# Performance work log

Hardware: AMD Instinct MI355X
Metric: run time of the kernel (lower is better)

Reference implementation:

```python
import jax, jax.numpy as jnp
import numpy as np

# ---- static config (mirrors init_kwargs + fixed setup box dims) ----
PC_MIN = jnp.array([0.0, -40.0, -3.0])
VOXEL_SIZE = jnp.array([0.05, 0.05, 0.1])
STRIDE = 4                     # pool_cfg.STRIDE and multi_scale_3d_strides['x_conv4']
EXTEND = 2.0                   # model_cfg.ROI_EXTEND_FACTOR
GRID_ZYX = (10, 400, 352)      # sparse spatial shape after stride-4 downsample [z,y,x]
# grid_size = round(extended_dims / voxel_size / STRIDE) for fixed dims [6.4,3.2,1.6]
GX, GY, GZ = 64, 32, 4
G = GX * GY * GZ
N_VOX, C = 200_000, 128
M = 64
KX, KY, KZ = 7, 7, 3


def setup_inputs() -> dict:
    key = jax.random.key(0)
    k1, k2, k3, k4, k5, k6, k7, k8, k9 = jax.random.split(key, 9)
    ctr = jnp.stack([
        jax.random.uniform(k1, (M,), minval=10.0, maxval=60.0),
        jax.random.uniform(k2, (M,), minval=-25.0, maxval=25.0),
        jax.random.uniform(k3, (M,), minval=-1.5, maxval=0.5)], axis=-1)
    dims = jnp.tile(jnp.array([[6.4, 3.2, 1.6]], jnp.float32), (M, 1))  # fixed -> static grid
    yaw = jax.random.uniform(k4, (M, 1), minval=-np.pi, maxval=np.pi)
    rois = jnp.concatenate([ctr, dims, yaw], axis=-1).astype(jnp.float32)
    proto_box = jnp.array([0.0, 0.0, 0.0, 6.4, 3.2, 1.6, 0.3], jnp.float32)
    voxel_feats = jax.random.normal(k5, (N_VOX, C), jnp.float32)
    feat_proto = jax.random.normal(k6, (1, KX, KY, KZ, C), jnp.float32) * 0.1
    zc = jax.random.randint(k7, (N_VOX,), 0, GRID_ZYX[0])
    yc = jax.random.randint(k8, (N_VOX,), 0, GRID_ZYX[1])
    xc = jax.random.randint(k9, (N_VOX,), 0, GRID_ZYX[2])
    voxel_coords = jnp.stack([jnp.zeros_like(zc), zc, yc, xc], -1).astype(jnp.int32)
    return dict(rois=rois, proto_box=proto_box, voxel_feats=voxel_feats,
                feat_proto=feat_proto, voxel_coords=voxel_coords)


def _dense_grid_points(box):
    # get_dense_grid_points: row-major (x,y,z) index order, matches torch nonzero()
    idx = jnp.stack(jnp.meshgrid(jnp.arange(GX), jnp.arange(GY), jnp.arange(GZ),
                                 indexing='ij'), -1).reshape(-1, 3).astype(jnp.float32)
    gs = jnp.array([GX, GY, GZ], jnp.float32)
    return (idx + 0.5) / gs * box[3:6] - box[3:6] / 2.0  # (G,3)


def _rotate_z(pts, ang):
    # common_utils.rotate_points_along_z: pts @ [[c,s,0],[-s,c,0],[0,0,1]]
    c, s = jnp.cos(ang), jnp.sin(ang)
    R = jnp.stack([jnp.stack([c, s, 0.0 * c]),
                   jnp.stack([-s, c, 0.0 * c]),
                   jnp.stack([0.0 * c, 0.0 * c, 1.0 + 0.0 * c])])
    return pts @ R


def reference(rois, proto_box, voxel_feats, feat_proto, voxel_coords):
    # generate_voxel2pinds: dense [Z,Y,X] grid of voxel row indices, -1 = empty
    v2p = -jnp.ones(GRID_ZYX, jnp.int32)
    v2p = v2p.at[voxel_coords[:, 1], voxel_coords[:, 2], voxel_coords[:, 3]].set(
        jnp.arange(N_VOX, dtype=jnp.int32))

    def per_roi(box):
        box = box.at[3:5].multiply(EXTEND)                 # xy_dim_extend
        local = _dense_grid_points(box)                    # (G,3)
        xyz = _rotate_z(local, box[6]) + box[:3]           # global roi grid points
        coords = jnp.floor((xyz - PC_MIN) / VOXEL_SIZE)    # '//' floor-div semantics
        coords = jnp.floor(coords / STRIDE).astype(jnp.int32)
        xc, yc, zc = coords[:, 0], coords[:, 1], coords[:, 2]
        inb = ((zc >= 0) & (zc < GRID_ZYX[0]) & (yc >= 0) & (yc < GRID_ZYX[1]) &
               (xc >= 0) & (xc < GRID_ZYX[2]))
        pidx = v2p[jnp.clip(zc, 0, GRID_ZYX[0] - 1),
                   jnp.clip(yc, 0, GRID_ZYX[1] - 1),
                   jnp.clip(xc, 0, GRID_ZYX[2] - 1)]
        valid = inb & (pidx >= 0)
        feat = jnp.where(valid[:, None], voxel_feats[jnp.clip(pidx, 0)], 0.0)  # (G,C)
        return feat, xyz

    feats, grid_xyz = jax.vmap(per_roi)(rois)              # (M,G,C), (M,G,3)
    vol = feats.reshape(M, GX, GY, GZ, C).transpose(0, 4, 1, 2, 3)   # NCDHW
    kern = feat_proto.transpose(0, 4, 1, 2, 3)                        # (1,C,KX,KY,KZ)
    pads = [(KX // 2,) * 2, (KY // 2,) * 2, (KZ // 2,) * 2]           # ceil((k-1)/2)
    mm = jax.lax.conv_general_dilated(vol, kern, (1, 1, 1), pads,
                                      dimension_numbers=('NCDHW', 'OIDHW', 'NCDHW'))
    # fresh BatchNorm3d(1) applied per-ROI (batch 1 each call): per-sample norm
    mu = jnp.mean(mm, axis=(1, 2, 3, 4), keepdims=True)
    var = jnp.var(mm, axis=(1, 2, 3, 4), keepdims=True)
    mm = (mm - mu) / jnp.sqrt(var + 1e-5)
    idx = jnp.minimum(jnp.argmax(mm.reshape(M, -1), axis=1), G - 1)
    sel = jnp.take_along_axis(grid_xyz, idx[:, None, None], axis=1)[:, 0, :]  # (M,3)
    rois_new = jnp.tile(proto_box[None], (M, 1))
    rois_new = rois_new.at[:, :3].set(sel)
    return rois_new
```

## Files before the change

kernel.cpp:

```cpp
#include <hip/hip_runtime.h>
#include <stdint.h>

#define GRID_Z 10
#define GRID_Y 400
#define GRID_X 352
#define NGRID (GRID_Z * GRID_Y * GRID_X)
#define NVOX 200000
#define CCH 128
#define MROI 64
#define GXD 64
#define GYD 32
#define GZD 4
#define GCELLS 8192
#define NTAPS 147
#define TROWS 32
#define NSLC 12
#define PITCH 136
#define NTT 10
#define BFRAGN (NTT * 4 * 64)

typedef short bf16x8 __attribute__((ext_vector_type(8)));
typedef float f32x4 __attribute__((ext_vector_type(4)));

__device__ __forceinline__ unsigned f2bf(float x) {
    unsigned u = __float_as_uint(x);
    return (u + 0x7FFFu + ((u >> 16) & 1u)) >> 16;
}
__device__ __forceinline__ float bf2f(unsigned h) {
    return __uint_as_float(h << 16);
}

__device__ __forceinline__ void cell_xyz(const float* __restrict__ roi, int g,
                                         float& X, float& Y, float& Z) {
#pragma clang fp contract(off)
    int iz = g & 3;
    int iy = (g >> 2) & 31;
    int ix = g >> 7;
    float bx = roi[3] * 2.0f;
    float by = roi[4] * 2.0f;
    float bz = roi[5];
    float lx = (ix + 0.5f) / 64.0f * bx - bx / 2.0f;
    float ly = (iy + 0.5f) / 32.0f * by - by / 2.0f;
    float lz = (iz + 0.5f) / 4.0f  * bz - bz / 2.0f;
    float c = cosf(roi[6]);
    float s = sinf(roi[6]);
    X = lx * c + ly * (-s) + roi[0];
    Y = lx * s + ly * c    + roi[1];
    Z = lz + roi[2];
}

__device__ __forceinline__ int cell_to_pidx(const float* __restrict__ roi, int g,
                                            const int* __restrict__ v2p) {
#pragma clang fp contract(off)
    float X, Y, Z;
    cell_xyz(roi, g, X, Y, Z);
    float fx = floorf((X - 0.0f)     / 0.05f);
    float fy = floorf((Y - (-40.0f)) / 0.05f);
    float fz = floorf((Z - (-3.0f))  / 0.1f);
    int cx = (int)floorf(fx / 4.0f);
    int cy = (int)floorf(fy / 4.0f);
    int cz = (int)floorf(fz / 4.0f);
    int p = -1;
    if (cz >= 0 && cz < GRID_Z && cy >= 0 && cy < GRID_Y && cx >= 0 && cx < GRID_X)
        p = v2p[(cz * GRID_Y + cy) * GRID_X + cx];
    return p;
}

__global__ void k_prep(const float* __restrict__ fproto,
                       uint4* __restrict__ bH, uint4* __restrict__ bL) {
    int tT   = blockIdx.x;
    int ks   = threadIdx.x >> 6;
    int lane = threadIdx.x & 63;
    int tap  = tT * 16 + (lane & 15);
    int k0   = ks * 32 + (lane >> 4) * 8;
    unsigned hi[8], lo[8];
    #pragma unroll
    for (int j = 0; j < 8; ++j) {
        float x = (tap < NTAPS) ? fproto[tap * CCH + k0 + j] : 0.0f;
        unsigned h = f2bf(x);
        float r = x - bf2f(h);
        hi[j] = h;
        lo[j] = f2bf(r);
    }
    uint4 uh, ul;
    uh.x = hi[0] | (hi[1] << 16); uh.y = hi[2] | (hi[3] << 16);
    uh.z = hi[4] | (hi[5] << 16); uh.w = hi[6] | (hi[7] << 16);
    ul.x = lo[0] | (lo[1] << 16); ul.y = lo[2] | (lo[3] << 16);
    ul.z = lo[4] | (lo[5] << 16); ul.w = lo[6] | (lo[7] << 16);
    int idx = (tT * 4 + ks) * 64 + lane;
    bH[idx] = uh;
    bL[idx] = ul;
}

__global__ void k_scatter(const int* __restrict__ vcoords, int* __restrict__ v2p,
                          int* __restrict__ cnt) {
    int i = blockIdx.x * 256 + threadIdx.x;
    if (blockIdx.x == 0 && threadIdx.x < MROI) cnt[threadIdx.x] = 0;
    if (i >= NVOX) return;
    int z = vcoords[i * 4 + 1];
    int y = vcoords[i * 4 + 2];
    int x = vcoords[i * 4 + 3];
    atomicMax(&v2p[(z * GRID_Y + y) * GRID_X + x], i);
}

__global__ void k_build(const float* __restrict__ rois, const int* __restrict__ v2p,
                        unsigned* __restrict__ list, int* __restrict__ cnt) {
    int g = blockIdx.x * 256 + threadIdx.x;
    int m = blockIdx.y;
    int lane = threadIdx.x & 63;
    int p = cell_to_pidx(rois + m * 7, g, v2p);
    bool v = p >= 0;
    unsigned long long bal = __ballot(v);
    int nset = __popcll(bal);
    int base = 0;
    if (lane == 0 && nset) base = atomicAdd(&cnt[m], nset);
    base = __shfl(base, 0, 64);
    if (v) {
        int pos = __popcll(bal & ((1ull << lane) - 1ull));
        list[m * GCELLS + base + pos] = ((unsigned)p << 13) | (unsigned)g;
    }
}

__global__ __launch_bounds__(256) void k_dots(
        const float* __restrict__ vfeat, const uint4* __restrict__ bH,
        const uint4* __restrict__ bL, const unsigned* __restrict__ list,
        const int* __restrict__ cnt, float* __restrict__ partial) {
    __shared__ float sscore[GCELLS];
    __shared__ __align__(16) unsigned short sAh[TROWS * PITCH];
    __shared__ __align__(16) unsigned short sAl[TROWS * PITCH];
    __shared__ unsigned sg[TROWS];

    const int m    = blockIdx.y;
    const int tid  = threadIdx.x;
    const int w    = tid >> 6;
    const int lane = tid & 63;
    const int rt   = w >> 1;
    const int th   = w & 1;
    const int col  = lane & 15;
    const int kg   = lane >> 4;
    const int n    = cnt[m];
    const unsigned* lst = list + m * GCELLS;

    int tkx[5], tky[5], tkz[5], tok[5];
    #pragma unroll
    for (int tt = 0; tt < 5; ++tt) {
        int t = th * 80 + tt * 16 + col;
        tok[tt] = t < NTAPS;
        int tc = tok[tt] ? t : 0;
        int kx  = tc / 21;
        int rem = tc - kx * 21;
        tkx[tt] = kx; tky[tt] = rem / 3; tkz[tt] = rem - tky[tt] * 3;
    }
    {
        float4* s4 = (float4*)sscore;
        #pragma unroll
        for (int i = 0; i < GCELLS / 4 / 256; ++i)
            s4[tid + 256 * i] = make_float4(0.f, 0.f, 0.f, 0.f);
    }
    for (int vt0 = blockIdx.x * TROWS; vt0 < n; vt0 += TROWS * NSLC) {
        __syncthreads();
        {
            int r = tid >> 3, q = tid & 7, v = vt0 + r;
            unsigned e = 0xFFFFFFFFu;
            if (v < n) e = lst[v];
            if (q == 0) sg[r] = e;
            if (e != 0xFFFFFFFFu) {
                int p = (int)(e >> 13);
                const float4* src = (const float4*)(vfeat + (size_t)p * CCH) + q * 4;
                unsigned hb[16], lb[16];
                #pragma unroll
                for (int j = 0; j < 4; ++j) {
                    float4 s = src[j];
                    float xs[4] = {s.x, s.y, s.z, s.w};
                    #pragma unroll
                    for (int c = 0; c < 4; ++c) {
                        unsigned h = f2bf(xs[c]);
                        hb[j * 4 + c] = h;
                        lb[j * 4 + c] = f2bf(xs[c] - bf2f(h));
                    }
                }
                uint4 h0, h1, l0, l1;
                h0.x = hb[0]  | (hb[1]  << 16); h0.y = hb[2]  | (hb[3]  << 16);
                h0.z = hb[4]  | (hb[5]  << 16); h0.w = hb[6]  | (hb[7]  << 16);
                h1.x = hb[8]  | (hb[9]  << 16); h1.y = hb[10] | (hb[11] << 16);
                h1.z = hb[12] | (hb[13] << 16); h1.w = hb[14] | (hb[15] << 16);
                l0.x = lb[0]  | (lb[1]  << 16); l0.y = lb[2]  | (lb[3]  << 16);
                l0.z = lb[4]  | (lb[5]  << 16); l0.w = lb[6]  | (lb[7]  << 16);
                l1.x = lb[8]  | (lb[9]  << 16); l1.y = lb[10] | (lb[11] << 16);
                l1.z = lb[12] | (lb[13] << 16); l1.w = lb[14] | (lb[15] << 16);
                uint4* dh = (uint4*)((char*)sAh + r * (PITCH * 2) + q * 32);
                uint4* dl = (uint4*)((char*)sAl + r * (PITCH * 2) + q * 32);
                dh[0] = h0; dh[1] = h1;
                dl[0] = l0; dl[1] = l1;
            }
        }
        __syncthreads();
        bf16x8 ah[4], al[4];
        const char* abh = (const char*)sAh + (rt * 16 + col) * (PITCH * 2);
        const char* abl = (const char*)sAl + (rt * 16 + col) * (PITCH * 2);
        #pragma unroll
        for (int ks = 0; ks < 4; ++ks) {
            ah[ks] = *(const bf16x8*)(abh + ks * 64 + kg * 16);
            al[ks] = *(const bf16x8*)(abl + ks * 64 + kg * 16);
        }
        f32x4 acc[5];
        #pragma unroll
        for (int tt = 0; tt < 5; ++tt) acc[tt] = (f32x4){0.f, 0.f, 0.f, 0.f};
        #pragma unroll
        for (int tt = 0; tt < 5; ++tt) {
            const int bi = ((th * 5 + tt) * 4) * 64 + lane;
            #pragma unroll
            for (int ks = 0; ks < 4; ++ks) {
                uint4 uh = bH[bi + ks * 64];
                uint4 ul = bL[bi + ks * 64];
                bf16x8 bh = *(bf16x8*)&uh;
                bf16x8 bl = *(bf16x8*)&ul;
                acc[tt] = __builtin_amdgcn_mfma_f32_16x16x32_bf16(ah[ks], bh, acc[tt], 0, 0, 0);
                acc[tt] = __builtin_amdgcn_mfma_f32_16x16x32_bf16(ah[ks], bl, acc[tt], 0, 0, 0);
                acc[tt] = __builtin_amdgcn_mfma_f32_16x16x32_bf16(al[ks], bh, acc[tt], 0, 0, 0);
            }
        }
        #pragma unroll
        for (int tt = 0; tt < 5; ++tt) {
            if (!tok[tt]) continue;
            #pragma unroll
            for (int rg = 0; rg < 4; ++rg) {
                unsigned e = sg[rt * 16 + kg * 4 + rg];
                if (e == 0xFFFFFFFFu) continue;
                int g  = (int)(e & 8191u);
                int cx = (g >> 7)        - (tkx[tt] - 3);
                int cy = ((g >> 2) & 31) - (tky[tt] - 3);
                int cz = (g & 3)         - (tkz[tt] - 1);
                if ((unsigned)cx < (unsigned)GXD && (unsigned)cy < (unsigned)GYD &&
                    (unsigned)cz < (unsigned)GZD)
                    atomicAdd(&sscore[(cx << 7) | (cy << 2) | cz], acc[tt][rg]);
            }
        }
    }
    __syncthreads();
    {
        float* dst = partial + ((size_t)m * NSLC + blockIdx.x) * GCELLS;
        const float4* s4 = (const float4*)sscore;
        float4* d4 = (float4*)dst;
        #pragma unroll
        for (int i = 0; i < GCELLS / 4 / 256; ++i)
            d4[tid + 256 * i] = s4[tid + 256 * i];
    }
}

__global__ __launch_bounds__(1024) void k_argfin(
        const float* __restrict__ partial, const float* __restrict__ rois,
        const float* __restrict__ pbox, float* __restrict__ out) {
    __shared__ unsigned long long red[1024];
    int m = blockIdx.x;
    int tid = threadIdx.x;
    const float* base = partial + (size_t)m * NSLC * GCELLS;
    unsigned long long bk = 0ull;
    #pragma unroll
    for (int i = 0; i < GCELLS / 1024; ++i) {
        int g = tid + 1024 * i;
        float v = 0.0f;
        #pragma unroll
        for (int s = 0; s < NSLC; ++s) v += base[s * GCELLS + g];
        unsigned ub  = __float_as_uint(v);
        unsigned key = (ub & 0x80000000u) ? ~ub : (ub | 0x80000000u);
        unsigned long long pk =
            ((unsigned long long)key << 32) | (unsigned)(GCELLS - 1 - g);
        bk = bk > pk ? bk : pk;
    }
    red[tid] = bk;
    __syncthreads();
    for (int s = 512; s > 0; s >>= 1) {
        if (tid < s) {
            unsigned long long o = red[tid + s];
            if (o > red[tid]) red[tid] = o;
        }
        __syncthreads();
    }
    if (tid == 0) {
        int g = (GCELLS - 1) - (int)(unsigned)(red[0] & 0xFFFFFFFFu);
        float X, Y, Z;
        cell_xyz(rois + m * 7, g, X, Y, Z);
        out[m * 7 + 0] = X;
        out[m * 7 + 1] = Y;
        out[m * 7 + 2] = Z;
        out[m * 7 + 3] = pbox[3];
        out[m * 7 + 4] = pbox[4];
        out[m * 7 + 5] = pbox[5];
        out[m * 7 + 6] = pbox[6];
    }
}

extern "C" void kernel_launch(void* const* d_in, const int* in_sizes, int n_in,
                              void* d_out, int out_size, void* d_ws, size_t ws_size,
                              hipStream_t stream) {
    const float* rois    = (const float*)d_in[0];
    const float* pbox    = (const float*)d_in[1];
    const float* vfeat   = (const float*)d_in[2];
    const float* fproto  = (const float*)d_in[3];
    const int*   vcoords = (const int*)d_in[4];
    float* out = (float*)d_out;

    int*      v2p     = (int*)d_ws;
    unsigned* list    = (unsigned*)(v2p + NGRID);
    float*    partial = (float*)(list + (size_t)MROI * GCELLS);
    uint4*    bH      = (uint4*)(partial + (size_t)NSLC * MROI * GCELLS);
    uint4*    bL      = bH + BFRAGN;
    int*      cnt     = (int*)(bL + BFRAGN);

    hipMemsetAsync(v2p, 0xFF, (size_t)NGRID * 4, stream);
    k_prep   <<<NTT, 256, 0, stream>>>(fproto, bH, bL);
    k_scatter<<<(NVOX + 255) / 256, 256, 0, stream>>>(vcoords, v2p, cnt);
    k_build  <<<dim3(GCELLS / 256, MROI), 256, 0, stream>>>(rois, v2p, list, cnt);
    k_dots   <<<dim3(NSLC, MROI), 256, 0, stream>>>(vfeat, bH, bL, list, cnt, partial);
    k_argfin <<<MROI, 1024, 0, stream>>>(partial, rois, pbox, out);
}
```

Before: 281.7 us.

## Fuse memset into prep kernel, hoist trig in build, split argmax across blocks

Replaces the hipMemsetAsync of the voxel-to-point map with int4 stores inside an enlarged prep kernel. That kernel also precomputes per-ROI cos/sin and resets the counters. The build kernel now has each thread handle one (x,y) column and loop over the 4 z cells, so the rotation math runs once per column. The final argmax is split across 16 blocks per ROI that merge through a global atomicMax, and the last block to finish, detected with a done counter, writes all outputs. The aim is to cut launch and serial overhead and to raise parallelism in the tail kernel, at the cost of grid-wide atomics and a last-block handoff.

```diff
diff --git a/kernel.cpp b/kernel.cpp
--- a/kernel.cpp
+++ b/kernel.cpp
@@ -18,6 +18,8 @@
 #define PITCH 136
 #define NTT 10
 #define BFRAGN (NTT * 4 * 64)
+#define VCLR ((NGRID / 4 + 255) / 256)
+#define ABLK 16
 
 typedef short bf16x8 __attribute__((ext_vector_type(8)));
 typedef float f32x4 __attribute__((ext_vector_type(4)));
@@ -49,53 +51,55 @@
     Z = lz + roi[2];
 }
 
-__device__ __forceinline__ int cell_to_pidx(const float* __restrict__ roi, int g,
-                                            const int* __restrict__ v2p) {
+__global__ void k_prep(const float* __restrict__ fproto, const float* __restrict__ rois,
+                       uint4* __restrict__ bH, uint4* __restrict__ bL,
+                       float2* __restrict__ rtrig, unsigned long long* __restrict__ best,
+                       int* __restrict__ cnt, unsigned* __restrict__ done,
+                       int* __restrict__ v2p) {
+    if (blockIdx.x < NTT) {
+        int tT   = blockIdx.x;
+        int ks   = threadIdx.x >> 6;
+        int lane = threadIdx.x & 63;
+        int tap  = tT * 16 + (lane & 15);
+        int k0   = ks * 32 + (lane >> 4) * 8;
+        unsigned hi[8], lo[8];
+        #pragma unroll
+        for (int j = 0; j < 8; ++j) {
+            float x = (tap < NTAPS) ? fproto[tap * CCH + k0 + j] : 0.0f;
+            unsigned h = f2bf(x);
+            float r = x - bf2f(h);
+            hi[j] = h;
+            lo[j] = f2bf(r);
+        }
+        uint4 uh, ul;
+        uh.x = hi[0] | (hi[1] << 16); uh.y = hi[2] | (hi[3] << 16);
+        uh.z = hi[4] | (hi[5] << 16); uh.w = hi[6] | (hi[7] << 16);
+        ul.x = lo[0] | (lo[1] << 16); ul.y = lo[2] | (lo[3] << 16);
+        ul.z = lo[4] | (lo[5] << 16); ul.w = lo[6] | (lo[7] << 16);
+        int idx = (tT * 4 + ks) * 64 + lane;
+        bH[idx] = uh;
+        bL[idx] = ul;
+    } else if (blockIdx.x == NTT) {
 #pragma clang fp contract(off)
-    float X, Y, Z;
-    cell_xyz(roi, g, X, Y, Z);
-    float fx = floorf((X - 0.0f)     / 0.05f);
-    float fy = floorf((Y - (-40.0f)) / 0.05f);
-    float fz = floorf((Z - (-3.0f))  / 0.1f);
-    int cx = (int)floorf(fx / 4.0f);
-    int cy = (int)floorf(fy / 4.0f);
-    int cz = (int)floorf(fz / 4.0f);
-    int p = -1;
-    if (cz >= 0 && cz < GRID_Z && cy >= 0 && cy < GRID_Y && cx >= 0 && cx < GRID_X)
-        p = v2p[(cz * GRID_Y + cy) * GRID_X + cx];
-    return p;
-}
-
-__global__ void k_prep(const float* __restrict__ fproto,
-                       uint4* __restrict__ bH, uint4* __restrict__ bL) {
-    int tT   = blockIdx.x;
-    int ks   = threadIdx.x >> 6;
-    int lane = threadIdx.x & 63;
-    int tap  = tT * 16 + (lane & 15);
-    int k0   = ks * 32 + (lane >> 4) * 8;
-    unsigned hi[8], lo[8];
-    #pragma unroll
-    for (int j = 0; j < 8; ++j) {
-        float x = (tap < NTAPS) ? fproto[tap * CCH + k0 + j] : 0.0f;
-        unsigned h = f2bf(x);
-        float r = x - bf2f(h);
-        hi[j] = h;
-        lo[j] = f2bf(r);
-    }
-    uint4 uh, ul;
-    uh.x = hi[0] | (hi[1] << 16); uh.y = hi[2] | (hi[3] << 16);
-    uh.z = hi[4] | (hi[5] << 16); uh.w = hi[6] | (hi[7] << 16);
-    ul.x = lo[0] | (lo[1] << 16); ul.y = lo[2] | (lo[3] << 16);
-    ul.z = lo[4] | (lo[5] << 16); ul.w = lo[6] | (lo[7] << 16);
-    int idx = (tT * 4 + ks) * 64 + lane;
-    bH[idx] = uh;
-    bL[idx] = ul;
-}
-
-__global__ void k_scatter(const int* __restrict__ vcoords, int* __restrict__ v2p,
-                          int* __restrict__ cnt) {
+        int t = threadIdx.x;
+        if (t < MROI) {
+            float yaw = rois[t * 7 + 6];
+            rtrig[t] = make_float2(cosf(yaw), sinf(yaw));
+            cnt[t] = 0;
+            best[t] = 0ull;
+        }
+        if (t == 0) *done = 0u;
+    } else {
+        int i = (blockIdx.x - NTT - 1) * 256 + threadIdx.x;
+        if (i < NGRID / 4) {
+            int4* p = (int4*)v2p;
+            p[i] = make_int4(-1, -1, -1, -1);
+        }
+    }
+}
+
+__global__ void k_scatter(const int* __restrict__ vcoords, int* __restrict__ v2p) {
     int i = blockIdx.x * 256 + threadIdx.x;
-    if (blockIdx.x == 0 && threadIdx.x < MROI) cnt[threadIdx.x] = 0;
     if (i >= NVOX) return;
     int z = vcoords[i * 4 + 1];
     int y = vcoords[i * 4 + 2];
@@ -103,21 +107,51 @@
     atomicMax(&v2p[(z * GRID_Y + y) * GRID_X + x], i);
 }
 
-__global__ void k_build(const float* __restrict__ rois, const int* __restrict__ v2p,
-                        unsigned* __restrict__ list, int* __restrict__ cnt) {
-    int g = blockIdx.x * 256 + threadIdx.x;
-    int m = blockIdx.y;
+__global__ void k_build(const float* __restrict__ rois, const float2* __restrict__ rtrig,
+                        const int* __restrict__ v2p, unsigned* __restrict__ list,
+                        int* __restrict__ cnt) {
+#pragma clang fp contract(off)
+    int m   = blockIdx.y;
+    int idx = blockIdx.x * 256 + threadIdx.x;
+    int ix  = idx >> 5;
+    int iy  = idx & 31;
     int lane = threadIdx.x & 63;
-    int p = cell_to_pidx(rois + m * 7, g, v2p);
-    bool v = p >= 0;
-    unsigned long long bal = __ballot(v);
-    int nset = __popcll(bal);
-    int base = 0;
-    if (lane == 0 && nset) base = atomicAdd(&cnt[m], nset);
-    base = __shfl(base, 0, 64);
-    if (v) {
-        int pos = __popcll(bal & ((1ull << lane) - 1ull));
-        list[m * GCELLS + base + pos] = ((unsigned)p << 13) | (unsigned)g;
+
+    const float* roi = rois + m * 7;
+    float c = rtrig[m].x, s = rtrig[m].y;
+    float bx = roi[3] * 2.0f;
+    float by = roi[4] * 2.0f;
+    float bz = roi[5];
+    float lx = (ix + 0.5f) / 64.0f * bx - bx / 2.0f;
+    float ly = (iy + 0.5f) / 32.0f * by - by / 2.0f;
+    float X = lx * c + ly * (-s) + roi[0];
+    float Y = lx * s + ly * c    + roi[1];
+    float fx = floorf((X - 0.0f)     / 0.05f);
+    float fy = floorf((Y - (-40.0f)) / 0.05f);
+    int cx = (int)floorf(fx / 4.0f);
+    int cy = (int)floorf(fy / 4.0f);
+    bool okxy = (cy >= 0 && cy < GRID_Y && cx >= 0 && cx < GRID_X);
+    int gbase = (ix << 7) | (iy << 2);
+
+    #pragma unroll
+    for (int iz = 0; iz < 4; ++iz) {
+        float lz = (iz + 0.5f) / 4.0f * bz - bz / 2.0f;
+        float Z  = lz + roi[2];
+        float fz = floorf((Z - (-3.0f)) / 0.1f);
+        int cz = (int)floorf(fz / 4.0f);
+        int p = -1;
+        if (okxy && cz >= 0 && cz < GRID_Z)
+            p = v2p[(cz * GRID_Y + cy) * GRID_X + cx];
+        bool v = p >= 0;
+        unsigned long long bal = __ballot(v);
+        int nset = __popcll(bal);
+        int base = 0;
+        if (lane == 0 && nset) base = atomicAdd(&cnt[m], nset);
+        base = __shfl(base, 0, 64);
+        if (v) {
+            int pos = __popcll(bal & ((1ull << lane) - 1ull));
+            list[m * GCELLS + base + pos] = ((unsigned)p << 13) | (unsigned)(gbase | iz);
+        }
     }
 }
 
@@ -248,46 +282,57 @@
     }
 }
 
-__global__ __launch_bounds__(1024) void k_argfin(
+__global__ __launch_bounds__(256) void k_argfin(
         const float* __restrict__ partial, const float* __restrict__ rois,
-        const float* __restrict__ pbox, float* __restrict__ out) {
-    __shared__ unsigned long long red[1024];
-    int m = blockIdx.x;
-    int tid = threadIdx.x;
+        const float* __restrict__ pbox, unsigned long long* __restrict__ best,
+        unsigned* __restrict__ done, float* __restrict__ out) {
+    __shared__ unsigned long long red[256];
+    __shared__ unsigned lastflag;
+    const int tid = threadIdx.x;
+    const int m = blockIdx.y;
     const float* base = partial + (size_t)m * NSLC * GCELLS;
+    const int c0 = blockIdx.x * (GCELLS / ABLK);
     unsigned long long bk = 0ull;
     #pragma unroll
-    for (int i = 0; i < GCELLS / 1024; ++i) {
-        int g = tid + 1024 * i;
+    for (int i = 0; i < GCELLS / ABLK / 256; ++i) {
+        int c = c0 + tid + 256 * i;
         float v = 0.0f;
         #pragma unroll
-        for (int s = 0; s < NSLC; ++s) v += base[s * GCELLS + g];
+        for (int s = 0; s < NSLC; ++s) v += base[s * GCELLS + c];
         unsigned ub  = __float_as_uint(v);
         unsigned key = (ub & 0x80000000u) ? ~ub : (ub | 0x80000000u);
         unsigned long long pk =
-            ((unsigned long long)key << 32) | (unsigned)(GCELLS - 1 - g);
+            ((unsigned long long)key << 32) | (unsigned)(GCELLS - 1 - c);
         bk = bk > pk ? bk : pk;
     }
     red[tid] = bk;
     __syncthreads();
-    for (int s = 512; s > 0; s >>= 1) {
-        if (tid < s) {
-            unsigned long long o = red[tid + s];
+    for (int st = 128; st > 0; st >>= 1) {
+        if (tid < st) {
+            unsigned long long o = red[tid + st];
             if (o > red[tid]) red[tid] = o;
         }
         __syncthreads();
     }
     if (tid == 0) {
-        int g = (GCELLS - 1) - (int)(unsigned)(red[0] & 0xFFFFFFFFu);
+        atomicMax(&best[m], red[0]);
+        __threadfence();
+        unsigned d = atomicAdd(done, 1u);
+        lastflag = (d == ABLK * MROI - 1u);
+    }
+    __syncthreads();
+    if (lastflag && tid < MROI) {
+        unsigned long long bv = atomicMax(&best[tid], 0ull);
+        int g = (GCELLS - 1) - (int)(unsigned)(bv & 0xFFFFFFFFu);
         float X, Y, Z;
-        cell_xyz(rois + m * 7, g, X, Y, Z);
-        out[m * 7 + 0] = X;
-        out[m * 7 + 1] = Y;
-        out[m * 7 + 2] = Z;
-        out[m * 7 + 3] = pbox[3];
-        out[m * 7 + 4] = pbox[4];
-        out[m * 7 + 5] = pbox[5];
-        out[m * 7 + 6] = pbox[6];
+        cell_xyz(rois + tid * 7, g, X, Y, Z);
+        out[tid * 7 + 0] = X;
+        out[tid * 7 + 1] = Y;
+        out[tid * 7 + 2] = Z;
+        out[tid * 7 + 3] = pbox[3];
+        out[tid * 7 + 4] = pbox[4];
+        out[tid * 7 + 5] = pbox[5];
+        out[tid * 7 + 6] = pbox[6];
     }
 }
 
@@ -306,12 +351,15 @@
     float*    partial = (float*)(list + (size_t)MROI * GCELLS);
     uint4*    bH      = (uint4*)(partial + (size_t)NSLC * MROI * GCELLS);
     uint4*    bL      = bH + BFRAGN;
-    int*      cnt     = (int*)(bL + BFRAGN);
-
-    hipMemsetAsync(v2p, 0xFF, (size_t)NGRID * 4, stream);
-    k_prep   <<<NTT, 256, 0, stream>>>(fproto, bH, bL);
-    k_scatter<<<(NVOX + 255) / 256, 256, 0, stream>>>(vcoords, v2p, cnt);
-    k_build  <<<dim3(GCELLS / 256, MROI), 256, 0, stream>>>(rois, v2p, list, cnt);
+    float2*   rtrig   = (float2*)(bL + BFRAGN);
+    unsigned long long* best = (unsigned long long*)(rtrig + MROI);
+    int*      cnt     = (int*)(best + MROI);
+    unsigned* done    = (unsigned*)(cnt + MROI);
+
+    k_prep   <<<NTT + 1 + VCLR, 256, 0, stream>>>(fproto, rois, bH, bL, rtrig,
+                                                  best, cnt, done, v2p);
+    k_scatter<<<(NVOX + 255) / 256, 256, 0, stream>>>(vcoords, v2p);
+    k_build  <<<dim3(8, MROI), 256, 0, stream>>>(rois, rtrig, v2p, list, cnt);
     k_dots   <<<dim3(NSLC, MROI), 256, 0, stream>>>(vfeat, bH, bL, list, cnt, partial);
-    k_argfin <<<MROI, 1024, 0, stream>>>(partial, rois, pbox, out);
-}
+    k_argfin <<<dim3(ABLK, MROI), 256, 0, stream>>>(partial, rois, pbox, best, done, out);
+}
```

New measurement: 283.0 us. No clear change (+0.5%).
